# Kernel optimization log

Measured on AMD Instinct MI355X. Metric: run time of the kernel, lower is better.

Reference implementation:

```python
import jax, jax.numpy as jnp
import numpy as np


def setup_inputs() -> dict:
    key = jax.random.key(0)
    k1, k2, k3, k4 = jax.random.split(key, 4)
    B, T, L, D = 16, 1024, 1024, 1024
    text_features = jax.random.normal(k1, (B, T, D), dtype=jnp.float32)
    local_features = jax.random.normal(k2, (B, L, D), dtype=jnp.float32)
    W_w = jax.random.normal(k3, (D, D), dtype=jnp.float32) * (1.0 / np.sqrt(D))
    W_b = jax.random.normal(k4, (D,), dtype=jnp.float32) * 0.01
    return {"text_features": text_features, "local_features": local_features, "W_w": W_w, "W_b": W_b}


def reference(text_features, local_features, W_w, W_b):
    # Linear projection: nn.Linear applies x @ W.T + b
    proj = jnp.einsum('btd,ed->bte', text_features, W_w) + W_b  # [B, T, D]
    # Bilinear cross-attention scores (no scaling, as in the original)
    scores = jnp.einsum('btd,bld->btl', proj, local_features)   # [B, T, L]
    attention_weights = jax.nn.softmax(scores, axis=2)
    weighted_local_features = jnp.einsum('btl,bld->btd', attention_weights, local_features)
    return weighted_local_features
```

## Files before the change

### kernel.cpp

```cpp
#include <hip/hip_runtime.h>
#include <hip/hip_fp16.h>

typedef _Float16 f16;
typedef _Float16 f16x8 __attribute__((ext_vector_type(8)));
typedef _Float16 f16x4 __attribute__((ext_vector_type(4)));
typedef float f32x4 __attribute__((ext_vector_type(4)));

#define DEV static __device__ __forceinline__
#define VMCNT(n) asm volatile("s_waitcnt vmcnt(" #n ")" ::: "memory")

DEV void barfence() {
    __builtin_amdgcn_s_barrier();
    asm volatile("" ::: "memory");
}

DEV void async_copy16(const f16* gsrc, f16* ldst) {
    __builtin_amdgcn_global_load_lds(
        (const __attribute__((address_space(1))) void*)gsrc,
        (__attribute__((address_space(3))) void*)ldst,
        16, 0, 0);
}

__global__ void convert_f16_k(const float* __restrict__ src, f16* __restrict__ dst, int n4) {
    for (int idx = blockIdx.x * 256 + threadIdx.x; idx < n4; idx += gridDim.x * 256) {
        float4 v = reinterpret_cast<const float4*>(src)[idx];
        f16x4 o;
        o[0] = (f16)v.x; o[1] = (f16)v.y; o[2] = (f16)v.z; o[3] = (f16)v.w;
        *reinterpret_cast<f16x4*>(dst + (size_t)idx * 4) = o;
    }
}

__global__ void split_local_k(const float* __restrict__ local,
                              f16* __restrict__ localF, f16* __restrict__ localT) {
    __shared__ float tile[64][65];
    const int b  = blockIdx.z;
    const int l0 = blockIdx.y * 64;
    const int d0 = blockIdx.x * 64;
    const int r  = threadIdx.x >> 4;
    const int c4 = threadIdx.x & 15;
    const float* src = local + ((size_t)b * 1024 + l0) * 1024 + d0;
    #pragma unroll
    for (int rr = 0; rr < 4; rr++) {
        int row = rr * 16 + r;
        float4 v = *reinterpret_cast<const float4*>(src + (size_t)row * 1024 + c4 * 4);
        float vv[4] = {v.x, v.y, v.z, v.w};
        f16x4 hv;
        #pragma unroll
        for (int e = 0; e < 4; e++) {
            tile[row][c4 * 4 + e] = vv[e];
            hv[e] = (f16)vv[e];
        }
        *reinterpret_cast<f16x4*>(localF + ((size_t)b * 1024 + l0 + row) * 1024 + d0 + c4 * 4) = hv;
    }
    __syncthreads();
    #pragma unroll
    for (int rr = 0; rr < 4; rr++) {
        int d = rr * 16 + r;
        f16x4 o;
        #pragma unroll
        for (int e = 0; e < 4; e++) o[e] = (f16)tile[c4 * 4 + e][d];
        *reinterpret_cast<f16x4*>(localT + ((size_t)b * 1024 + d0 + d) * 1024 + l0 + c4 * 4) = o;
    }
}

DEV void load_af(const f16* lds, int base, int c0, int c1, f16x8 (&a)[4][2]) {
    #pragma unroll
    for (int i = 0; i < 4; i++) {
        a[i][0] = *reinterpret_cast<const f16x8*>(&lds[base + i * 1024 + c0]);
        a[i][1] = *reinterpret_cast<const f16x8*>(&lds[base + i * 1024 + c1]);
    }
}
DEV void load_bf(const f16* lds, int base, int c0, int c1, f16x8 (&b)[2][2]) {
    #pragma unroll
    for (int j = 0; j < 2; j++) {
        b[j][0] = *reinterpret_cast<const f16x8*>(&lds[base + j * 1024 + c0]);
        b[j][1] = *reinterpret_cast<const f16x8*>(&lds[base + j * 1024 + c1]);
    }
}
template <int Q>
DEV void mfma16(const f16x8 (&a)[4][2], const f16x8 (&b)[2][2], f32x4 (&acc)[4][4][2]) {
    __builtin_amdgcn_s_setprio(1);
    #pragma unroll
    for (int i = 0; i < 4; i++)
        #pragma unroll
        for (int j = 0; j < 2; j++) {
            acc[Q][i][j] = __builtin_amdgcn_mfma_f32_16x16x32_f16(a[i][0], b[j][0], acc[Q][i][j], 0, 0, 0);
            acc[Q][i][j] = __builtin_amdgcn_mfma_f32_16x16x32_f16(a[i][1], b[j][1], acc[Q][i][j], 0, 0, 0);
        }
    __builtin_amdgcn_s_setprio(0);
}

template <int EPI>
__launch_bounds__(512)
__global__ void gemm256_k(const f16* __restrict__ A, const f16* __restrict__ B,
                          float* __restrict__ Cf, f16* __restrict__ Cs,
                          const float* __restrict__ bias,
                          int N, int K, long sA, long sB, long sC, int nbn) {
    extern __shared__ f16 lds[];
    const int nwg  = gridDim.x;
    const int cpx  = nwg >> 3;
    const int wgid = (blockIdx.x & 7) * cpx + (blockIdx.x >> 3);
    const int per_b = (EPI == 0) ? nwg : 16;
    const int bz  = wgid / per_b;
    const int rem = wgid % per_b;
    const int bm  = rem / nbn;
    const int bn  = rem % nbn;

    const int tid  = threadIdx.x;
    const int lane = tid & 63;
    const int w    = tid >> 6;
    const int wr   = w >> 2, wc = w & 3;
    const f16* Ab = A + (size_t)bz * sA + (size_t)(bm * 256) * K;
    const f16* Bb = B + (size_t)bz * sB + (size_t)(bn * 256) * K;
    const int rloc = lane >> 3;
    const int sl8  = ((lane & 7) ^ rloc) * 8;
    const int lrow = lane & 15;
    const int c0 = (8 * (lane >> 4)) ^ (8 * (lane & 7));
    const int c1 = c0 ^ 32;
    const int abase = (wr * 64 + lrow) * 64;
    const int bbase = (wc * 32 + lrow) * 64;

    auto stageA = [&](int sb, int half, int k0) {
        #pragma unroll
        for (int i = 0; i < 2; i++) {
            int rr = (w * 2 + i) * 8 + rloc;
            async_copy16(Ab + (size_t)(half * 128 + rr) * K + k0 + sl8,
                         &lds[sb + half * 8192 + (w * 2 + i) * 512 + lane * 8]);
        }
    };
    auto stageB = [&](int sb, int half, int k0) {
        #pragma unroll
        for (int i = 0; i < 2; i++) {
            int rr = (w * 2 + i) * 8 + rloc;
            async_copy16(Bb + (size_t)(half * 128 + rr) * K + k0 + sl8,
                         &lds[sb + 16384 + half * 8192 + (w * 2 + i) * 512 + lane * 8]);
        }
    };

    f32x4 acc[4][4][2] = {};
    const int nt = K >> 6;

    stageA(0, 0, 0); stageB(0, 0, 0);
    stageB(0, 1, 0); stageA(0, 1, 0);
    VMCNT(4);
    barfence();

    for (int t = 0; t < nt - 1; ++t) {
        const int cb = (t & 1) * 32768;
        const int sb = cb ^ 32768;
        const int kn = (t + 1) * 64;
        f16x8 af[4][2], bf0[2][2], bf1[2][2];
        load_af(lds, cb + abase, c0, c1, af);
        load_bf(lds, cb + 16384 + bbase, c0, c1, bf0);
        stageA(sb, 0, kn); stageB(sb, 0, kn);
        barfence();
        mfma16<0>(af, bf0, acc);
        VMCNT(6);
        barfence();
        load_bf(lds, cb + 16384 + 8192 + bbase, c0, c1, bf1);
        stageB(sb, 1, kn);
        barfence();
        mfma16<1>(af, bf1, acc);
        VMCNT(6);
        barfence();
        load_af(lds, cb + 8192 + abase, c0, c1, af);
        stageA(sb, 1, kn);
        barfence();
        mfma16<2>(af, bf0, acc);
        mfma16<3>(af, bf1, acc);
        VMCNT(4);
        barfence();
    }
    {
        const int cb = ((nt - 1) & 1) * 32768;
        f16x8 af[4][2], bf0[2][2], bf1[2][2];
        load_af(lds, cb + abase, c0, c1, af);
        load_bf(lds, cb + 16384 + bbase, c0, c1, bf0);
        barfence();
        mfma16<0>(af, bf0, acc);
        VMCNT(2);
        barfence();
        load_bf(lds, cb + 16384 + 8192 + bbase, c0, c1, bf1);
        barfence();
        mfma16<1>(af, bf1, acc);
        VMCNT(0);
        barfence();
        load_af(lds, cb + 8192 + abase, c0, c1, af);
        barfence();
        mfma16<2>(af, bf0, acc);
        mfma16<3>(af, bf1, acc);
    }

    const int r4 = (lane >> 4) * 4, cl = lane & 15;
    #pragma unroll
    for (int q = 0; q < 4; q++)
        #pragma unroll
        for (int i = 0; i < 4; i++)
            #pragma unroll
            for (int j = 0; j < 2; j++) {
                const int row0 = bm * 256 + (q >> 1) * 128 + wr * 64 + i * 16 + r4;
                const int col  = bn * 256 + (q & 1) * 128 + wc * 32 + j * 16 + cl;
                if constexpr (EPI == 0) {
                    float bv = bias[col];
                    #pragma unroll
                    for (int r = 0; r < 4; r++) {
                        float v = acc[q][i][j][r] + bv;
                        Cs[(size_t)(row0 + r) * N + col] = (f16)v;
                    }
                } else {
                    #pragma unroll
                    for (int r = 0; r < 4; r++)
                        Cf[(size_t)bz * sC + (size_t)(row0 + r) * N + col] = acc[q][i][j][r];
                }
            }
}

__global__ void softmax_k(const float* __restrict__ S, f16* __restrict__ P) {
    __shared__ float red[8];
    const int row = blockIdx.x;
    const int t = threadIdx.x;
    const int wv = t >> 6, ln = t & 63;
    float4 v = reinterpret_cast<const float4*>(S + (size_t)row * 1024)[t];
    float m = fmaxf(fmaxf(v.x, v.y), fmaxf(v.z, v.w));
    #pragma unroll
    for (int off = 1; off < 64; off <<= 1) m = fmaxf(m, __shfl_xor(m, off));
    if (ln == 0) red[wv] = m;
    __syncthreads();
    m = fmaxf(fmaxf(red[0], red[1]), fmaxf(red[2], red[3]));
    float e0 = __expf(v.x - m), e1 = __expf(v.y - m), e2 = __expf(v.z - m), e3 = __expf(v.w - m);
    float s = e0 + e1 + e2 + e3;
    #pragma unroll
    for (int off = 1; off < 64; off <<= 1) s += __shfl_xor(s, off);
    if (ln == 0) red[4 + wv] = s;
    __syncthreads();
    s = red[4] + red[5] + red[6] + red[7];
    float inv = 1.0f / s;
    f16x4 o;
    o[0] = (f16)(e0 * inv); o[1] = (f16)(e1 * inv); o[2] = (f16)(e2 * inv); o[3] = (f16)(e3 * inv);
    *reinterpret_cast<f16x4*>(P + (size_t)row * 1024 + t * 4) = o;
}

extern "C" void kernel_launch(void* const* d_in, const int* in_sizes, int n_in,
                              void* d_out, int out_size, void* d_ws, size_t ws_size,
                              hipStream_t stream) {
    const float* text  = (const float*)d_in[0];
    const float* local = (const float*)d_in[1];
    const float* Ww    = (const float*)d_in[2];
    const float* Wb    = (const float*)d_in[3];
    float* out = (float*)d_out;

    char* ws = (char*)d_ws;
    const size_t MB = 1024 * 1024;
    f16*   textF  = (f16*)(ws);
    f16*   WF     = (f16*)(ws + 32 * MB);
    f16*   localF = (f16*)(ws + 36 * MB);
    f16*   localT = (f16*)(ws + 68 * MB);
    f16*   projF  = (f16*)(ws + 100 * MB);
    float* scores = (float*)(ws + 132 * MB);
    f16*   attn   = (f16*)(ws);

    auto g0 = gemm256_k<0>;
    auto g1 = gemm256_k<1>;
    (void)hipFuncSetAttribute((const void*)g0, hipFuncAttributeMaxDynamicSharedMemorySize, 131072);
    (void)hipFuncSetAttribute((const void*)g1, hipFuncAttributeMaxDynamicSharedMemorySize, 131072);

    hipLaunchKernelGGL(convert_f16_k, dim3(2048), dim3(256), 0, stream, text, textF, 16384 * 256);
    hipLaunchKernelGGL(convert_f16_k, dim3(512), dim3(256), 0, stream, Ww, WF, 1024 * 256);
    hipLaunchKernelGGL(split_local_k, dim3(16, 16, 16), dim3(256), 0, stream,
                       local, localF, localT);
    hipLaunchKernelGGL(g0, dim3(256), dim3(512), 131072, stream,
                       textF, WF, (float*)nullptr, projF, Wb,
                       1024, 1024, 0L, 0L, 0L, 4);
    hipLaunchKernelGGL(g1, dim3(256), dim3(512), 131072, stream,
                       projF, localF, scores, (f16*)nullptr, (const float*)nullptr,
                       1024, 1024, (long)1024 * 1024, (long)1024 * 1024, (long)1024 * 1024, 4);
    hipLaunchKernelGGL(softmax_k, dim3(16384), dim3(256), 0, stream, scores, attn);
    hipLaunchKernelGGL(g1, dim3(256), dim3(512), 131072, stream,
                       attn, localT, out, (f16*)nullptr, (const float*)nullptr,
                       1024, 1024, (long)1024 * 1024, (long)1024 * 1024, (long)1024 * 1024, 4);
}
```

Baseline: 309.2 us.

## Fuse score GEMM with row softmax in a full-row tile kernel

Replaces the score GEMM (fp32 scores written to workspace) and the separate softmax kernel with one kernel. Each workgroup computes a 64x1024 score tile that covers whole rows, then does max, exp and sum reductions in registers and LDS, and writes fp16 attention weights directly. This removes the 64MB fp32 scores write and its read-back, plus one launch. The cost is a narrower 64-row tile with 4-byte async copies for A, which may lower MFMA efficiency and data reuse compared with the 256x256 GEMM.

```diff
diff --git a/kernel.cpp b/kernel.cpp
--- a/kernel.cpp
+++ b/kernel.cpp
@@ -19,6 +19,12 @@
         (const __attribute__((address_space(1))) void*)gsrc,
         (__attribute__((address_space(3))) void*)ldst,
         16, 0, 0);
+}
+DEV void async_copy4(const f16* gsrc, f16* ldst) {
+    __builtin_amdgcn_global_load_lds(
+        (const __attribute__((address_space(1))) void*)gsrc,
+        (__attribute__((address_space(3))) void*)ldst,
+        4, 0, 0);
 }
 
 __global__ void convert_f16_k(const float* __restrict__ src, f16* __restrict__ dst, int n4) {
@@ -215,29 +221,159 @@
             }
 }
 
-__global__ void softmax_k(const float* __restrict__ S, f16* __restrict__ P) {
-    __shared__ float red[8];
-    const int row = blockIdx.x;
-    const int t = threadIdx.x;
-    const int wv = t >> 6, ln = t & 63;
-    float4 v = reinterpret_cast<const float4*>(S + (size_t)row * 1024)[t];
-    float m = fmaxf(fmaxf(v.x, v.y), fmaxf(v.z, v.w));
-    #pragma unroll
-    for (int off = 1; off < 64; off <<= 1) m = fmaxf(m, __shfl_xor(m, off));
-    if (ln == 0) red[wv] = m;
-    __syncthreads();
-    m = fmaxf(fmaxf(red[0], red[1]), fmaxf(red[2], red[3]));
-    float e0 = __expf(v.x - m), e1 = __expf(v.y - m), e2 = __expf(v.z - m), e3 = __expf(v.w - m);
-    float s = e0 + e1 + e2 + e3;
-    #pragma unroll
-    for (int off = 1; off < 64; off <<= 1) s += __shfl_xor(s, off);
-    if (ln == 0) red[4 + wv] = s;
-    __syncthreads();
-    s = red[4] + red[5] + red[6] + red[7];
-    float inv = 1.0f / s;
-    f16x4 o;
-    o[0] = (f16)(e0 * inv); o[1] = (f16)(e1 * inv); o[2] = (f16)(e2 * inv); o[3] = (f16)(e3 * inv);
-    *reinterpret_cast<f16x4*>(P + (size_t)row * 1024 + t * 4) = o;
+DEV void mfma_q(const f16x8 (&a)[4], const f16x8 (&b)[4], f32x4 (&acc)[4][8], int h) {
+    __builtin_amdgcn_s_setprio(1);
+    #pragma unroll
+    for (int i = 0; i < 4; i++)
+        #pragma unroll
+        for (int jj = 0; jj < 4; jj++)
+            acc[i][h * 4 + jj] = __builtin_amdgcn_mfma_f32_16x16x32_f16(a[i], b[jj], acc[i][h * 4 + jj], 0, 0, 0);
+    __builtin_amdgcn_s_setprio(0);
+}
+
+__launch_bounds__(512)
+__global__ void fused_sm_k(const f16* __restrict__ projF, const f16* __restrict__ localF,
+                           f16* __restrict__ attn) {
+    extern __shared__ f16 lds[];
+    const int wgid = (blockIdx.x & 7) * 32 + (blockIdx.x >> 3);
+    const int bz = wgid >> 4, bm = wgid & 15;
+    const int tid = threadIdx.x, lane = tid & 63, w = tid >> 6;
+    const int lrow = lane & 15, lslot = lane >> 4;
+    const f16* Pa = projF + ((size_t)bz * 1024 + bm * 64) * 1024;
+    const f16* Lb = localF + (size_t)bz * 1024 * 1024;
+    const int BUF = 34816;
+
+    auto stageA = [&](int sb, int k0) {
+        #pragma unroll
+        for (int q = 0; q < 2; q++) {
+            int row = q * 32 + (tid >> 4);
+            int s   = (tid >> 2) & 3;
+            int w2  = (tid & 3) * 2;
+            async_copy4(Pa + (size_t)row * 1024 + k0 + (s ^ ((row >> 1) & 3)) * 8 + w2,
+                        &lds[sb + q * 1024 + tid * 2]);
+        }
+    };
+    auto stageB = [&](int sb, int h, int k0) {
+        #pragma unroll
+        for (int q = 0; q < 4; q++) {
+            int widx = q * 128 + (tid >> 2);
+            int r    = (widx >> 6) * 128 + h * 64 + (widx & 63);
+            int slot = tid & 3;
+            async_copy16(Lb + (size_t)r * 1024 + k0 + ((slot ^ ((r >> 1) & 3)) * 8),
+                         &lds[sb + 2048 + h * 16384 + q * 4096 + tid * 8]);
+        }
+    };
+    auto ldA = [&](int cb, f16x8 (&a)[4]) {
+        #pragma unroll
+        for (int i = 0; i < 4; i++) {
+            int row = i * 16 + lrow;
+            a[i] = *reinterpret_cast<const f16x8*>(
+                &lds[cb + row * 32 + ((lslot ^ ((row >> 1) & 3)) * 8)]);
+        }
+    };
+    auto ldB = [&](int cb, int h, f16x8 (&b)[4]) {
+        #pragma unroll
+        for (int jj = 0; jj < 4; jj++) {
+            int r    = w * 128 + h * 64 + jj * 16 + lrow;
+            int widx = w * 64 + jj * 16 + lrow;
+            b[jj] = *reinterpret_cast<const f16x8*>(
+                &lds[cb + 2048 + h * 16384 + widx * 32 + ((lslot ^ ((r >> 1) & 3)) * 8)]);
+        }
+    };
+
+    f32x4 acc[4][8] = {};
+
+    stageA(0, 0); stageB(0, 0, 0); stageB(0, 1, 0);
+    VMCNT(4);
+    barfence();
+
+    for (int t = 0; t < 31; ++t) {
+        const int cb = (t & 1) * BUF, sb = cb ^ BUF;
+        const int kn = (t + 1) * 32;
+        f16x8 a[4], b[4];
+        ldA(cb, a); ldB(cb, 0, b);
+        stageA(sb, kn); stageB(sb, 0, kn);
+        barfence();
+        mfma_q(a, b, acc, 0);
+        VMCNT(6);
+        barfence();
+        ldB(cb, 1, b);
+        stageB(sb, 1, kn);
+        barfence();
+        mfma_q(a, b, acc, 1);
+        VMCNT(4);
+        barfence();
+    }
+    {
+        const int cb = BUF;
+        f16x8 a[4], b[4];
+        ldA(cb, a); ldB(cb, 0, b);
+        barfence();
+        mfma_q(a, b, acc, 0);
+        VMCNT(0);
+        barfence();
+        ldB(cb, 1, b);
+        barfence();
+        mfma_q(a, b, acc, 1);
+    }
+
+    barfence();
+    float* red = (float*)lds;
+    #pragma unroll
+    for (int i = 0; i < 4; i++)
+        #pragma unroll
+        for (int rr = 0; rr < 4; rr++) {
+            float m = acc[i][0][rr];
+            #pragma unroll
+            for (int j = 1; j < 8; j++) m = fmaxf(m, acc[i][j][rr]);
+            #pragma unroll
+            for (int off = 1; off < 16; off <<= 1) m = fmaxf(m, __shfl_xor(m, off));
+            if (lrow == 0) red[(i * 16 + lslot * 4 + rr) * 8 + w] = m;
+        }
+    barfence();
+    if (tid < 64) {
+        float m = red[tid * 8];
+        #pragma unroll
+        for (int k = 1; k < 8; k++) m = fmaxf(m, red[tid * 8 + k]);
+        red[512 + tid] = m;
+    }
+    barfence();
+    #pragma unroll
+    for (int i = 0; i < 4; i++)
+        #pragma unroll
+        for (int rr = 0; rr < 4; rr++) {
+            int row = i * 16 + lslot * 4 + rr;
+            float fm = red[512 + row];
+            float s = 0.f;
+            #pragma unroll
+            for (int j = 0; j < 8; j++) {
+                float e = __expf(acc[i][j][rr] - fm);
+                acc[i][j][rr] = e;
+                s += e;
+            }
+            #pragma unroll
+            for (int off = 1; off < 16; off <<= 1) s += __shfl_xor(s, off);
+            if (lrow == 0) red[row * 8 + w] = s;
+        }
+    barfence();
+    if (tid < 64) {
+        float s = 0.f;
+        #pragma unroll
+        for (int k = 0; k < 8; k++) s += red[tid * 8 + k];
+        red[576 + tid] = 1.0f / s;
+    }
+    barfence();
+    f16* Ob = attn + ((size_t)bz * 1024 + bm * 64) * 1024;
+    #pragma unroll
+    for (int i = 0; i < 4; i++)
+        #pragma unroll
+        for (int rr = 0; rr < 4; rr++) {
+            int row = i * 16 + lslot * 4 + rr;
+            float inv = red[576 + row];
+            #pragma unroll
+            for (int j = 0; j < 8; j++)
+                Ob[(size_t)row * 1024 + w * 128 + j * 16 + lrow] = (f16)(acc[i][j][rr] * inv);
+        }
 }
 
 extern "C" void kernel_launch(void* const* d_in, const int* in_sizes, int n_in,
@@ -251,18 +387,18 @@
 
     char* ws = (char*)d_ws;
     const size_t MB = 1024 * 1024;
-    f16*   textF  = (f16*)(ws);
-    f16*   WF     = (f16*)(ws + 32 * MB);
-    f16*   localF = (f16*)(ws + 36 * MB);
-    f16*   localT = (f16*)(ws + 68 * MB);
-    f16*   projF  = (f16*)(ws + 100 * MB);
-    float* scores = (float*)(ws + 132 * MB);
-    f16*   attn   = (f16*)(ws);
+    f16* textF  = (f16*)(ws);
+    f16* WF     = (f16*)(ws + 32 * MB);
+    f16* localF = (f16*)(ws + 36 * MB);
+    f16* localT = (f16*)(ws + 68 * MB);
+    f16* projF  = (f16*)(ws + 100 * MB);
+    f16* attn   = (f16*)(ws + 132 * MB);
 
     auto g0 = gemm256_k<0>;
     auto g1 = gemm256_k<1>;
     (void)hipFuncSetAttribute((const void*)g0, hipFuncAttributeMaxDynamicSharedMemorySize, 131072);
     (void)hipFuncSetAttribute((const void*)g1, hipFuncAttributeMaxDynamicSharedMemorySize, 131072);
+    (void)hipFuncSetAttribute((const void*)fused_sm_k, hipFuncAttributeMaxDynamicSharedMemorySize, 139264);
 
     hipLaunchKernelGGL(convert_f16_k, dim3(2048), dim3(256), 0, stream, text, textF, 16384 * 256);
     hipLaunchKernelGGL(convert_f16_k, dim3(512), dim3(256), 0, stream, Ww, WF, 1024 * 256);
@@ -271,10 +407,8 @@
     hipLaunchKernelGGL(g0, dim3(256), dim3(512), 131072, stream,
                        textF, WF, (float*)nullptr, projF, Wb,
                        1024, 1024, 0L, 0L, 0L, 4);
-    hipLaunchKernelGGL(g1, dim3(256), dim3(512), 131072, stream,
-                       projF, localF, scores, (f16*)nullptr, (const float*)nullptr,
-                       1024, 1024, (long)1024 * 1024, (long)1024 * 1024, (long)1024 * 1024, 4);
-    hipLaunchKernelGGL(softmax_k, dim3(16384), dim3(256), 0, stream, scores, attn);
+    hipLaunchKernelGGL(fused_sm_k, dim3(256), dim3(512), 139264, stream,
+                       projF, localF, attn);
     hipLaunchKernelGGL(g1, dim3(256), dim3(512), 131072, stream,
                        attn, localT, out, (f16*)nullptr, (const float*)nullptr,
                        1024, 1024, (long)1024 * 1024, (long)1024 * 1024, (long)1024 * 1024, 4);
```

Result: no change. 310.3 us (+0.4%).
